# Kernel optimization log

Hardware: AMD Instinct MI355X
Metric: run time of the kernel (lower is better)

The kernel has to match this reference:

```python
import jax, jax.numpy as jnp
import numpy as np

N_POINTS = 300000
N_PAIRS = 100000  # rulebook pairs per kernel offset
K_OFFSETS = 27    # 3x3x3 kernel
C_IN, C_OUT = 32, 64
GROUPS = 8
EPS = 1e-5
NEG_SLOPE = 0.01


def setup_inputs() -> dict:
    key = jax.random.key(0)
    k1, k2, k3, k4 = jax.random.split(key, 4)
    feats = jax.random.normal(k1, (N_POINTS, C_IN), dtype=jnp.float32)
    weight = jax.random.normal(k2, (K_OFFSETS, C_IN, C_OUT), dtype=jnp.float32) * (1.0 / np.sqrt(C_IN * K_OFFSETS))
    gamma = jnp.ones((C_OUT,), dtype=jnp.float32)
    beta = jnp.zeros((C_OUT,), dtype=jnp.float32)
    in_idx = jax.random.randint(k3, (K_OFFSETS, N_PAIRS), 0, N_POINTS, dtype=jnp.int64)
    out_idx = jax.random.randint(k4, (K_OFFSETS, N_PAIRS), 0, N_POINTS, dtype=jnp.int64)
    return {"feats": feats, "weight": weight, "gamma": gamma, "beta": beta,
            "in_idx": in_idx, "out_idx": out_idx}


def reference(feats, weight, gamma, beta, in_idx, out_idx):
    # Sparse 3D conv via rulebook: gather -> per-offset matmul -> scatter-add
    gathered = feats[in_idx]                       # [K, P, C_in]
    y = jnp.einsum('kpi,kio->kpo', gathered, weight)  # [K, P, C_out]
    out = jnp.zeros((feats.shape[0], weight.shape[2]), feats.dtype)
    out = out.at[out_idx.reshape(-1)].add(y.reshape(-1, weight.shape[2]))
    # GroupNorm(8, C_out): stats over all points and channels within each group
    N, C = out.shape
    xg = out.reshape(N, GROUPS, C // GROUPS)
    mean = jnp.mean(xg, axis=(0, 2), keepdims=True)
    var = jnp.var(xg, axis=(0, 2), keepdims=True)
    xn = ((xg - mean) * jax.lax.rsqrt(var + EPS)).reshape(N, C)
    xn = xn * gamma + beta
    # LeakyReLU (default negative_slope = 0.01)
    return jnp.where(xn >= 0, xn, NEG_SLOPE * xn)
```

## Files before the change

kernel.cpp:

```cpp
#include <hip/hip_runtime.h>

#define NPTS   300000
#define NPAIRS 100000
#define KOFF   27
#define CIN    32
#define COUT   64
#define NGROUP 8
#define EPSV   1e-5f
#define SLOPE  0.01f

#define PAIRS_PER_BLOCK 256
#define BLOCKS_PER_K ((NPAIRS + PAIRS_PER_BLOCK - 1) / PAIRS_PER_BLOCK)

__global__ __launch_bounds__(256) void zero_kernel(float4* __restrict__ out4, int n4,
                                                   float* __restrict__ stats) {
    int i = blockIdx.x * blockDim.x + threadIdx.x;
    if (i < n4) out4[i] = make_float4(0.f, 0.f, 0.f, 0.f);
    if (blockIdx.x == 0 && threadIdx.x < 16) stats[threadIdx.x] = 0.f;
}

__global__ __launch_bounds__(256) void conv_kernel(
    const float* __restrict__ feats, const float* __restrict__ weight,
    const int* __restrict__ in_idx, const int* __restrict__ out_idx,
    float* __restrict__ out)
{
    const int lane = threadIdx.x & 63;
    const int wave = threadIdx.x >> 6;
    const int k     = blockIdx.x / BLOCKS_PER_K;
    const int pair0 = (blockIdx.x % BLOCKS_PER_K) * PAIRS_PER_BLOCK;

    float w[CIN];
    const float* wk = weight + k * (CIN * COUT) + lane;
#pragma unroll
    for (int i = 0; i < CIN; ++i) w[i] = wk[i * COUT];

    const int per_wave = PAIRS_PER_BLOCK / 4;
    int p    = pair0 + wave * per_wave;
    int pend = p + per_wave;
    if (pend > NPAIRS) pend = NPAIRS;

    const int* ii = in_idx  + k * NPAIRS;
    const int* oi = out_idx + k * NPAIRS;

    for (; p < pend; ++p) {
        int rin  = __builtin_amdgcn_readfirstlane(ii[p]);
        int rout = __builtin_amdgcn_readfirstlane(oi[p]);
        const float* frow = feats + (size_t)rin * CIN;
        float acc = 0.f;
#pragma unroll
        for (int i = 0; i < CIN; ++i)
            acc = fmaf(frow[i], w[i], acc);
        atomicAdd(out + (size_t)rout * COUT + lane, acc);
    }
}

__global__ __launch_bounds__(256) void stats_kernel(const float* __restrict__ out,
                                                    float* __restrict__ stats) {
    const int c = threadIdx.x & 63;
    const int wave_in_grid = blockIdx.x * 4 + (threadIdx.x >> 6);
    const int nwaves = gridDim.x * 4;
    float s = 0.f, ss = 0.f;
    for (int r = wave_in_grid; r < NPTS; r += nwaves) {
        float v = out[(size_t)r * COUT + c];
        s += v; ss += v * v;
    }
#pragma unroll
    for (int m = 1; m < 8; m <<= 1) {
        s  += __shfl_xor(s,  m, 64);
        ss += __shfl_xor(ss, m, 64);
    }
    if ((c & 7) == 0) {
        int g = c >> 3;
        atomicAdd(stats + g,     s);
        atomicAdd(stats + 8 + g, ss);
    }
}

__global__ __launch_bounds__(256) void norm_kernel(float4* __restrict__ out4, int n4,
                                                   const float* __restrict__ stats,
                                                   const float* __restrict__ gamma,
                                                   const float* __restrict__ beta) {
    int i = blockIdx.x * blockDim.x + threadIdx.x;
    if (i >= n4) return;
    int c0 = (i & 15) * 4;
    int g  = c0 >> 3;
    const float cnt = (float)NPTS * (COUT / NGROUP);
    float mean = stats[g] / cnt;
    float var  = stats[8 + g] / cnt - mean * mean;
    float inv  = rsqrtf(var + EPSV);
    float4 v  = out4[i];
    float4 ga = *(const float4*)(gamma + c0);
    float4 be = *(const float4*)(beta  + c0);
    float x;
    x = (v.x - mean) * inv * ga.x + be.x; v.x = x >= 0.f ? x : SLOPE * x;
    x = (v.y - mean) * inv * ga.y + be.y; v.y = x >= 0.f ? x : SLOPE * x;
    x = (v.z - mean) * inv * ga.z + be.z; v.z = x >= 0.f ? x : SLOPE * x;
    x = (v.w - mean) * inv * ga.w + be.w; v.w = x >= 0.f ? x : SLOPE * x;
    out4[i] = v;
}

extern "C" void kernel_launch(void* const* d_in, const int* in_sizes, int n_in,
                              void* d_out, int out_size, void* d_ws, size_t ws_size,
                              hipStream_t stream) {
    const float* feats  = (const float*)d_in[0];
    const float* weight = (const float*)d_in[1];
    const float* gamma  = (const float*)d_in[2];
    const float* beta   = (const float*)d_in[3];
    const int*   in_idx = (const int*)d_in[4];
    const int*   out_idx= (const int*)d_in[5];
    float* out   = (float*)d_out;
    float* stats = (float*)d_ws;

    int n4 = out_size / 4;
    int zb = (n4 + 255) / 256;

    zero_kernel<<<zb, 256, 0, stream>>>((float4*)out, n4, stats);
    conv_kernel<<<KOFF * BLOCKS_PER_K, 256, 0, stream>>>(feats, weight, in_idx, out_idx, out);
    stats_kernel<<<1024, 256, 0, stream>>>(out, stats);
    norm_kernel<<<zb, 256, 0, stream>>>((float4*)out, n4, stats, gamma, beta);
}
```

Before: 823.5 us.

## Prefetch next feature row in conv loop and vectorize GroupNorm stats reduction

The conv loop now loads the feature row for the next rulebook pair while computing the current one, so the gather latency can overlap the FMAs and the atomic scatter. It also splits the dot product into two accumulators. The stats kernel reads float4s across the flat output, reduces by group with shuffles and a small LDS block reduction, and issues only 16 atomics per block. This costs extra registers for the second feature row and may lower occupancy in the atomic-heavy conv kernel.

```diff
diff --git a/kernel.cpp b/kernel.cpp
--- a/kernel.cpp
+++ b/kernel.cpp
@@ -38,41 +38,79 @@
     int p    = pair0 + wave * per_wave;
     int pend = p + per_wave;
     if (pend > NPAIRS) pend = NPAIRS;
+    if (p >= pend) return;
 
     const int* ii = in_idx  + k * NPAIRS;
     const int* oi = out_idx + k * NPAIRS;
 
-    for (; p < pend; ++p) {
-        int rin  = __builtin_amdgcn_readfirstlane(ii[p]);
+    int rin0 = __builtin_amdgcn_readfirstlane(ii[p]);
+    const float* f0 = feats + (size_t)rin0 * CIN;
+    float a[CIN];
+#pragma unroll
+    for (int i = 0; i < CIN; ++i) a[i] = f0[i];
+
+    for (; p + 1 < pend; ++p) {
+        int rin1 = __builtin_amdgcn_readfirstlane(ii[p + 1]);
+        const float* f1 = feats + (size_t)rin1 * CIN;
+        float b[CIN];
+#pragma unroll
+        for (int i = 0; i < CIN; ++i) b[i] = f1[i];
+
         int rout = __builtin_amdgcn_readfirstlane(oi[p]);
-        const float* frow = feats + (size_t)rin * CIN;
-        float acc = 0.f;
+        float acc0 = 0.f, acc1 = 0.f;
 #pragma unroll
-        for (int i = 0; i < CIN; ++i)
-            acc = fmaf(frow[i], w[i], acc);
-        atomicAdd(out + (size_t)rout * COUT + lane, acc);
+        for (int i = 0; i < CIN; i += 2) {
+            acc0 = fmaf(a[i],     w[i],     acc0);
+            acc1 = fmaf(a[i + 1], w[i + 1], acc1);
+        }
+        atomicAdd(out + (size_t)rout * COUT + lane, acc0 + acc1);
+
+#pragma unroll
+        for (int i = 0; i < CIN; ++i) a[i] = b[i];
+    }
+    {
+        int rout = __builtin_amdgcn_readfirstlane(oi[p]);
+        float acc0 = 0.f, acc1 = 0.f;
+#pragma unroll
+        for (int i = 0; i < CIN; i += 2) {
+            acc0 = fmaf(a[i],     w[i],     acc0);
+            acc1 = fmaf(a[i + 1], w[i + 1], acc1);
+        }
+        atomicAdd(out + (size_t)rout * COUT + lane, acc0 + acc1);
     }
 }
 
-__global__ __launch_bounds__(256) void stats_kernel(const float* __restrict__ out,
+__global__ __launch_bounds__(256) void stats_kernel(const float4* __restrict__ out4,
                                                     float* __restrict__ stats) {
-    const int c = threadIdx.x & 63;
-    const int wave_in_grid = blockIdx.x * 4 + (threadIdx.x >> 6);
-    const int nwaves = gridDim.x * 4;
+    const int tid  = blockIdx.x * 256 + threadIdx.x;
+    const int ntid = gridDim.x * 256;
+    const int n4   = NPTS * COUT / 4;
+
     float s = 0.f, ss = 0.f;
-    for (int r = wave_in_grid; r < NPTS; r += nwaves) {
-        float v = out[(size_t)r * COUT + c];
-        s += v; ss += v * v;
+    for (int i = tid; i < n4; i += ntid) {
+        float4 v = out4[i];
+        s  += v.x + v.y + v.z + v.w;
+        ss += v.x * v.x + v.y * v.y + v.z * v.z + v.w * v.w;
     }
+    s  += __shfl_xor(s,  1, 64);  ss += __shfl_xor(ss,  1, 64);
+    s  += __shfl_xor(s, 16, 64);  ss += __shfl_xor(ss, 16, 64);
+    s  += __shfl_xor(s, 32, 64);  ss += __shfl_xor(ss, 32, 64);
+
+    __shared__ float sm_s[4][NGROUP];
+    __shared__ float sm_ss[4][NGROUP];
+    const int lane = threadIdx.x & 63;
+    const int wv   = threadIdx.x >> 6;
+    if (lane < 16 && (lane & 1) == 0) {
+        sm_s [wv][lane >> 1] = s;
+        sm_ss[wv][lane >> 1] = ss;
+    }
+    __syncthreads();
+    if (threadIdx.x < NGROUP) {
+        float ts = 0.f, tss = 0.f;
 #pragma unroll
-    for (int m = 1; m < 8; m <<= 1) {
-        s  += __shfl_xor(s,  m, 64);
-        ss += __shfl_xor(ss, m, 64);
-    }
-    if ((c & 7) == 0) {
-        int g = c >> 3;
-        atomicAdd(stats + g,     s);
-        atomicAdd(stats + 8 + g, ss);
+        for (int wvi = 0; wvi < 4; ++wvi) { ts += sm_s[wvi][threadIdx.x]; tss += sm_ss[wvi][threadIdx.x]; }
+        atomicAdd(stats + threadIdx.x,          ts);
+        atomicAdd(stats + NGROUP + threadIdx.x, tss);
     }
 }
 
@@ -116,6 +154,6 @@
 
     zero_kernel<<<zb, 256, 0, stream>>>((float4*)out, n4, stats);
     conv_kernel<<<KOFF * BLOCKS_PER_K, 256, 0, stream>>>(feats, weight, in_idx, out_idx, out);
-    stats_kernel<<<1024, 256, 0, stream>>>(out, stats);
+    stats_kernel<<<2048, 256, 0, stream>>>((const float4*)out, stats);
     norm_kernel<<<zb, 256, 0, stream>>>((float4*)out, n4, stats, gamma, beta);
 }
```

Measured after the change: 769.5 us. 6.6% less time.
